# Performance work log

Hardware: AMD Instinct MI355X
Metric: run time of the kernel (lower is better)

Reference implementation:

```python
import jax, jax.numpy as jnp
import numpy as np
import math


def setup_inputs() -> dict:
    key = jax.random.key(0)
    k1, k2, k3 = jax.random.split(key, 3)
    b, h, w = 4, 64, 64
    hw = h * w
    gp_dim = 64
    sim_matrix = jax.random.normal(k1, (b, hw, hw), dtype=jnp.float32)
    conv_w = jax.random.normal(k2, (gp_dim, 2), dtype=jnp.float32)
    conv_b = jax.random.normal(k3, (gp_dim,), dtype=jnp.float32)
    return {"sim_matrix": sim_matrix, "conv_w": conv_w, "conv_b": conv_b,
            "b": b, "h": h, "w": w}


def _pos_enc(conv_w, conv_b, b, h, w):
    # normalized grid coords in (-1, 1), channel 0 = x (width), channel 1 = y (height)
    ys = jnp.linspace(-1.0 + 1.0 / h, 1.0 - 1.0 / h, h, dtype=jnp.float32)
    xs = jnp.linspace(-1.0 + 1.0 / w, 1.0 - 1.0 / w, w, dtype=jnp.float32)
    gy, gx = jnp.meshgrid(ys, xs, indexing="ij")          # [h, w] each
    coords = jnp.stack([gx, gy], axis=0)                   # [2, h, w]
    # 1x1 conv == per-pixel linear: [d,2] @ [2,h,w] + bias
    proj = jnp.einsum("dc,chw->dhw", conv_w, coords) + conv_b[:, None, None]
    f = jnp.cos(8.0 * math.pi * proj)                       # fourier basis, [d, h, w]
    return jnp.broadcast_to(f[None], (b,) + f.shape)        # [b, d, h, w]


def reference(sim_matrix, conv_w, conv_b, b, h, w):
    d = conv_w.shape[0]
    f = _pos_enc(conv_w, conv_b, b, h, w)                   # [b, d, h, w]
    f = f.reshape(b, d, h * w).transpose(0, 2, 1)           # [b, hw, d]
    conf = jax.nn.softmax(sim_matrix, axis=2)               # [b, hw, hw]
    gp = jnp.einsum("bnm,bmd->bnd", conf, f)                # [b, hw, d]
    return gp.transpose(0, 2, 1).reshape(b, d, h, w)        # [b, d, h, w]
```

## Files before the change

### kernel.cpp

```cpp
#include <hip/hip_runtime.h>


typedef _Float16 f16;
typedef f16 f16x8 __attribute__((ext_vector_type(8)));
typedef float f32x4 __attribute__((ext_vector_type(4)));

static constexpr int HW = 4096;
static constexpr int ND = 64;

__global__ __launch_bounds__(256) void posenc_f16(
    const float* __restrict__ cw, const float* __restrict__ cb,
    f16* __restrict__ ft)
{
    int g = blockIdx.x * 256 + threadIdx.x;
    int d = g >> 12;
    int m = g & 4095;
    int i = m >> 6;
    int j = m & 63;
    float gx = (float)(2 * j - 63) * (1.0f / 64.0f);
    float gy = (float)(2 * i - 63) * (1.0f / 64.0f);
    float proj = cw[2 * d] * gx + cw[2 * d + 1] * gy + cb[d];
    float v = cosf(25.132741228718345f * proj);
    ft[(size_t)d * HW + m] = (f16)v;
}

__global__ __launch_bounds__(256) void gp_main(
    const float* __restrict__ sim, const f16* __restrict__ ft,
    float* __restrict__ out)
{
    const int bb   = blockIdx.x >> 6;
    const int nt   = blockIdx.x & 63;
    const int wv   = threadIdx.x >> 6;
    const int lane = threadIdx.x & 63;
    const int c    = lane & 15;
    const int q    = lane >> 4;
    const int n0   = nt * 64 + wv * 16;

    const float* srow  = sim + (size_t)bb * HW * HW + (size_t)(n0 + c) * HW + q * 8;
    const f16*   fbase = ft + (size_t)c * HW + q * 8;

    f32x4 acc0 = {0.f, 0.f, 0.f, 0.f};
    f32x4 acc1 = {0.f, 0.f, 0.f, 0.f};
    f32x4 acc2 = {0.f, 0.f, 0.f, 0.f};
    f32x4 acc3 = {0.f, 0.f, 0.f, 0.f};
    float psum = 0.0f;

    #pragma unroll 2
    for (int m0 = 0; m0 < HW; m0 += 32) {
        f32x4 s0 = *(const f32x4*)(srow + m0);
        f32x4 s1 = *(const f32x4*)(srow + m0 + 4);

        float p0 = __expf(s0[0]);
        float p1 = __expf(s0[1]);
        float p2 = __expf(s0[2]);
        float p3 = __expf(s0[3]);
        float p4 = __expf(s1[0]);
        float p5 = __expf(s1[1]);
        float p6 = __expf(s1[2]);
        float p7 = __expf(s1[3]);
        psum += ((p0 + p1) + (p2 + p3)) + ((p4 + p5) + (p6 + p7));

        f16x8 a;
        a[0] = (f16)p0; a[1] = (f16)p1; a[2] = (f16)p2; a[3] = (f16)p3;
        a[4] = (f16)p4; a[5] = (f16)p5; a[6] = (f16)p6; a[7] = (f16)p7;

        f16x8 b0 = *(const f16x8*)(fbase + (size_t)(0 * 16) * HW + m0);
        f16x8 b1 = *(const f16x8*)(fbase + (size_t)(1 * 16) * HW + m0);
        f16x8 b2 = *(const f16x8*)(fbase + (size_t)(2 * 16) * HW + m0);
        f16x8 b3 = *(const f16x8*)(fbase + (size_t)(3 * 16) * HW + m0);

        acc0 = __builtin_amdgcn_mfma_f32_16x16x32_f16(a, b0, acc0, 0, 0, 0);
        acc1 = __builtin_amdgcn_mfma_f32_16x16x32_f16(a, b1, acc1, 0, 0, 0);
        acc2 = __builtin_amdgcn_mfma_f32_16x16x32_f16(a, b2, acc2, 0, 0, 0);
        acc3 = __builtin_amdgcn_mfma_f32_16x16x32_f16(a, b3, acc3, 0, 0, 0);
    }

    psum += __shfl_xor(psum, 16, 64);
    psum += __shfl_xor(psum, 32, 64);
    float r0 = 1.0f / __shfl(psum, q * 4 + 0, 64);
    float r1 = 1.0f / __shfl(psum, q * 4 + 1, 64);
    float r2 = 1.0f / __shfl(psum, q * 4 + 2, 64);
    float r3 = 1.0f / __shfl(psum, q * 4 + 3, 64);

    float* ob = out + (size_t)bb * ND * HW + (size_t)c * HW + n0 + q * 4;
    {
        f32x4 v; v[0] = acc0[0] * r0; v[1] = acc0[1] * r1; v[2] = acc0[2] * r2; v[3] = acc0[3] * r3;
        *(f32x4*)(ob + (size_t)(0 * 16) * HW) = v;
    }
    {
        f32x4 v; v[0] = acc1[0] * r0; v[1] = acc1[1] * r1; v[2] = acc1[2] * r2; v[3] = acc1[3] * r3;
        *(f32x4*)(ob + (size_t)(1 * 16) * HW) = v;
    }
    {
        f32x4 v; v[0] = acc2[0] * r0; v[1] = acc2[1] * r1; v[2] = acc2[2] * r2; v[3] = acc2[3] * r3;
        *(f32x4*)(ob + (size_t)(2 * 16) * HW) = v;
    }
    {
        f32x4 v; v[0] = acc3[0] * r0; v[1] = acc3[1] * r1; v[2] = acc3[2] * r2; v[3] = acc3[3] * r3;
        *(f32x4*)(ob + (size_t)(3 * 16) * HW) = v;
    }
}

extern "C" void kernel_launch(void* const* d_in, const int* in_sizes, int n_in,
                              void* d_out, int out_size, void* d_ws, size_t ws_size,
                              hipStream_t stream) {
    (void)in_sizes; (void)n_in; (void)out_size; (void)ws_size;
    const float* sim = (const float*)d_in[0];
    const float* cw  = (const float*)d_in[1];
    const float* cb  = (const float*)d_in[2];
    float* out = (float*)d_out;
    f16* ft = (f16*)d_ws;

    posenc_f16<<<(ND * HW) / 256, 256, 0, stream>>>(cw, cb, ft);
    gp_main<<<256, 256, 0, stream>>>(sim, ft, out);
}
```

Baseline: 393.2 us.

## Split softmax-GEMM reduction across eight waves with shared-memory combine

Each block now covers 16 rows instead of 64, and its eight waves each take one eighth of the 4096-wide reduction dimension. Partial MFMA accumulators and exp sums are combined through shared memory before the normalised result is written. This gives 1024 blocks of 512 threads instead of 256 blocks of 256, so more waves are in flight to hide memory latency on the bandwidth-bound stream of the 256MB sim matrix. The cost is a shared-memory reduction, a block barrier, and each wave reading its positional-encoding slice once per block.

```diff
diff --git a/kernel.cpp b/kernel.cpp
--- a/kernel.cpp
+++ b/kernel.cpp
@@ -7,6 +7,8 @@
 
 static constexpr int HW = 4096;
 static constexpr int ND = 64;
+static constexpr int KW = 8;
+static constexpr int KM = HW / KW;
 
 __global__ __launch_bounds__(256) void posenc_f16(
     const float* __restrict__ cw, const float* __restrict__ cb,
@@ -24,20 +26,21 @@
     ft[(size_t)d * HW + m] = (f16)v;
 }
 
-__global__ __launch_bounds__(256) void gp_main(
+__global__ __launch_bounds__(512) void gp_main(
     const float* __restrict__ sim, const f16* __restrict__ ft,
     float* __restrict__ out)
 {
-    const int bb   = blockIdx.x >> 6;
-    const int nt   = blockIdx.x & 63;
+    const int bb   = blockIdx.x >> 8;
+    const int nt   = blockIdx.x & 255;
     const int wv   = threadIdx.x >> 6;
     const int lane = threadIdx.x & 63;
     const int c    = lane & 15;
     const int q    = lane >> 4;
-    const int n0   = nt * 64 + wv * 16;
+    const int n0   = nt * 16;
 
-    const float* srow  = sim + (size_t)bb * HW * HW + (size_t)(n0 + c) * HW + q * 8;
-    const f16*   fbase = ft + (size_t)c * HW + q * 8;
+    const float* srow  = sim + (size_t)bb * HW * HW + (size_t)(n0 + c) * HW
+                             + wv * KM + q * 8;
+    const f16*   fbase = ft + (size_t)c * HW + wv * KM + q * 8;
 
     f32x4 acc0 = {0.f, 0.f, 0.f, 0.f};
     f32x4 acc1 = {0.f, 0.f, 0.f, 0.f};
@@ -45,8 +48,8 @@
     f32x4 acc3 = {0.f, 0.f, 0.f, 0.f};
     float psum = 0.0f;
 
-    #pragma unroll 2
-    for (int m0 = 0; m0 < HW; m0 += 32) {
+    #pragma unroll 4
+    for (int m0 = 0; m0 < KM; m0 += 32) {
         f32x4 s0 = *(const f32x4*)(srow + m0);
         f32x4 s1 = *(const f32x4*)(srow + m0 + 4);
 
@@ -75,29 +78,44 @@
         acc3 = __builtin_amdgcn_mfma_f32_16x16x32_f16(a, b3, acc3, 0, 0, 0);
     }
 
-    psum += __shfl_xor(psum, 16, 64);
-    psum += __shfl_xor(psum, 32, 64);
-    float r0 = 1.0f / __shfl(psum, q * 4 + 0, 64);
-    float r1 = 1.0f / __shfl(psum, q * 4 + 1, 64);
-    float r2 = 1.0f / __shfl(psum, q * 4 + 2, 64);
-    float r3 = 1.0f / __shfl(psum, q * 4 + 3, 64);
+    __shared__ f32x4 red[4][KW][64];
+    __shared__ float redsum[KW][64];
+    red[0][wv][lane] = acc0;
+    red[1][wv][lane] = acc1;
+    red[2][wv][lane] = acc2;
+    red[3][wv][lane] = acc3;
+    redsum[wv][lane] = psum;
+    __syncthreads();
 
-    float* ob = out + (size_t)bb * ND * HW + (size_t)c * HW + n0 + q * 4;
-    {
-        f32x4 v; v[0] = acc0[0] * r0; v[1] = acc0[1] * r1; v[2] = acc0[2] * r2; v[3] = acc0[3] * r3;
-        *(f32x4*)(ob + (size_t)(0 * 16) * HW) = v;
-    }
-    {
-        f32x4 v; v[0] = acc1[0] * r0; v[1] = acc1[1] * r1; v[2] = acc1[2] * r2; v[3] = acc1[3] * r3;
-        *(f32x4*)(ob + (size_t)(1 * 16) * HW) = v;
-    }
-    {
-        f32x4 v; v[0] = acc2[0] * r0; v[1] = acc2[1] * r1; v[2] = acc2[2] * r2; v[3] = acc2[3] * r3;
-        *(f32x4*)(ob + (size_t)(2 * 16) * HW) = v;
-    }
-    {
-        f32x4 v; v[0] = acc3[0] * r0; v[1] = acc3[1] * r1; v[2] = acc3[2] * r2; v[3] = acc3[3] * r3;
-        *(f32x4*)(ob + (size_t)(3 * 16) * HW) = v;
+    if (wv < 2) {
+        const int t0 = wv * 2, t1 = wv * 2 + 1;
+        f32x4 A0 = {0.f, 0.f, 0.f, 0.f};
+        f32x4 A1 = {0.f, 0.f, 0.f, 0.f};
+        float ps = 0.0f;
+        #pragma unroll
+        for (int s = 0; s < KW; s++) {
+            A0 += red[t0][s][lane];
+            A1 += red[t1][s][lane];
+            ps += redsum[s][lane];
+        }
+        ps += __shfl_xor(ps, 16, 64);
+        ps += __shfl_xor(ps, 32, 64);
+        float r0 = 1.0f / __shfl(ps, q * 4 + 0, 64);
+        float r1 = 1.0f / __shfl(ps, q * 4 + 1, 64);
+        float r2 = 1.0f / __shfl(ps, q * 4 + 2, 64);
+        float r3 = 1.0f / __shfl(ps, q * 4 + 3, 64);
+
+        float* ob = out + (size_t)bb * ND * HW + (size_t)c * HW + n0 + q * 4;
+        {
+            f32x4 v; v[0] = A0[0] * r0; v[1] = A0[1] * r1;
+                     v[2] = A0[2] * r2; v[3] = A0[3] * r3;
+            *(f32x4*)(ob + (size_t)t0 * 16 * HW) = v;
+        }
+        {
+            f32x4 v; v[0] = A1[0] * r0; v[1] = A1[1] * r1;
+                     v[2] = A1[2] * r2; v[3] = A1[3] * r3;
+            *(f32x4*)(ob + (size_t)t1 * 16 * HW) = v;
+        }
     }
 }
 
@@ -112,5 +130,5 @@
     f16* ft = (f16*)d_ws;
 
     posenc_f16<<<(ND * HW) / 256, 256, 0, stream>>>(cw, cb, ft);
-    gp_main<<<256, 256, 0, stream>>>(sim, ft, out);
+    gp_main<<<1024, 512, 0, stream>>>(sim, ft, out);
 }
```

New measurement: 384.1 us. -2.3%, faster.

## Stage sim and feature tiles through double-buffered LDS with 8-wave blocks

Applied to the files above, without the earlier changes.

Replaces per-lane strided global reads with cooperative coalesced loads of 64x128 sim tiles and 64x128 feature tiles into double-buffered shared memory, prefetching the next tile into registers while computing. Blocks grow to 8 waves, each handling 16 rows by 32 output channels, so exp is recomputed by two waves per row group. Row sums are combined via shared memory before normalization. This aims to improve memory coalescing and latency hiding at the cost of more LDS usage, barriers, and duplicated exp work.

```diff
diff --git a/kernel.cpp b/kernel.cpp
--- a/kernel.cpp
+++ b/kernel.cpp
@@ -5,8 +5,11 @@
 typedef f16 f16x8 __attribute__((ext_vector_type(8)));
 typedef float f32x4 __attribute__((ext_vector_type(4)));
 
-static constexpr int HW = 4096;
-static constexpr int ND = 64;
+static constexpr int HW  = 4096;
+static constexpr int ND  = 64;
+static constexpr int BK  = 128;
+static constexpr int AST = 132;
+static constexpr int BST = 136;
 
 __global__ __launch_bounds__(256) void posenc_f16(
     const float* __restrict__ cw, const float* __restrict__ cb,
@@ -24,81 +27,124 @@
     ft[(size_t)d * HW + m] = (f16)v;
 }
 
-__global__ __launch_bounds__(256) void gp_main(
+__global__ __launch_bounds__(512, 2) void gp_main(
     const float* __restrict__ sim, const f16* __restrict__ ft,
     float* __restrict__ out)
 {
     const int bb   = blockIdx.x >> 6;
-    const int nt   = blockIdx.x & 63;
-    const int wv   = threadIdx.x >> 6;
-    const int lane = threadIdx.x & 63;
+    const int ng   = blockIdx.x & 63;
+    const int n0   = ng * 64;
+    const int tid  = threadIdx.x;
+    const int wv   = tid >> 6;
+    const int lane = tid & 63;
     const int c    = lane & 15;
     const int q    = lane >> 4;
-    const int n0   = nt * 64 + wv * 16;
+    const int s    = wv & 3;
+    const int h    = wv >> 2;
 
-    const float* srow  = sim + (size_t)bb * HW * HW + (size_t)(n0 + c) * HW + q * 8;
-    const f16*   fbase = ft + (size_t)c * HW + q * 8;
+    __shared__ float As[2][64 * AST];
+    __shared__ f16   Bs[2][64 * BST];
+    __shared__ float Ls[64];
+
+    const float* simb = sim + (size_t)bb * HW * HW + (size_t)n0 * HW;
+
+    const int sr   = tid >> 5;
+    const int sc4  = tid & 31;
+    const int fd   = tid >> 4;
+    const int ft16 = tid & 15;
+
+    f32x4 sreg[4];
+    f16x8 freg[2];
+
+    #define LOAD_TILE(kt)                                                     \
+        {                                                                     \
+            const float* g = simb + (kt) * BK;                                \
+            _Pragma("unroll")                                                 \
+            for (int p = 0; p < 4; p++)                                       \
+                sreg[p] = *(const f32x4*)(g + (size_t)(p * 16 + sr) * HW      \
+                                            + sc4 * 4);                       \
+            const f16* gf = ft + (kt) * BK;                                   \
+            _Pragma("unroll")                                                 \
+            for (int p = 0; p < 2; p++)                                       \
+                freg[p] = *(const f16x8*)(gf + (size_t)(p * 32 + fd) * HW     \
+                                             + ft16 * 8);                     \
+        }
 
     f32x4 acc0 = {0.f, 0.f, 0.f, 0.f};
     f32x4 acc1 = {0.f, 0.f, 0.f, 0.f};
-    f32x4 acc2 = {0.f, 0.f, 0.f, 0.f};
-    f32x4 acc3 = {0.f, 0.f, 0.f, 0.f};
     float psum = 0.0f;
 
-    #pragma unroll 2
-    for (int m0 = 0; m0 < HW; m0 += 32) {
-        f32x4 s0 = *(const f32x4*)(srow + m0);
-        f32x4 s1 = *(const f32x4*)(srow + m0 + 4);
+    LOAD_TILE(0);
 
-        float p0 = __expf(s0[0]);
-        float p1 = __expf(s0[1]);
-        float p2 = __expf(s0[2]);
-        float p3 = __expf(s0[3]);
-        float p4 = __expf(s1[0]);
-        float p5 = __expf(s1[1]);
-        float p6 = __expf(s1[2]);
-        float p7 = __expf(s1[3]);
-        psum += ((p0 + p1) + (p2 + p3)) + ((p4 + p5) + (p6 + p7));
+    for (int kt = 0; kt < HW / BK; kt++) {
+        const int buf = kt & 1;
+        #pragma unroll
+        for (int p = 0; p < 4; p++)
+            *(f32x4*)&As[buf][(p * 16 + sr) * AST + sc4 * 4] = sreg[p];
+        #pragma unroll
+        for (int p = 0; p < 2; p++)
+            *(f16x8*)&Bs[buf][(p * 32 + fd) * BST + ft16 * 8] = freg[p];
+        __syncthreads();
 
-        f16x8 a;
-        a[0] = (f16)p0; a[1] = (f16)p1; a[2] = (f16)p2; a[3] = (f16)p3;
-        a[4] = (f16)p4; a[5] = (f16)p5; a[6] = (f16)p6; a[7] = (f16)p7;
+        if (kt < HW / BK - 1)
+            LOAD_TILE(kt + 1);
 
-        f16x8 b0 = *(const f16x8*)(fbase + (size_t)(0 * 16) * HW + m0);
-        f16x8 b1 = *(const f16x8*)(fbase + (size_t)(1 * 16) * HW + m0);
-        f16x8 b2 = *(const f16x8*)(fbase + (size_t)(2 * 16) * HW + m0);
-        f16x8 b3 = *(const f16x8*)(fbase + (size_t)(3 * 16) * HW + m0);
+        const float* as  = &As[buf][(s * 16 + c) * AST];
+        const f16*   bs0 = &Bs[buf][(h * 32 + c) * BST];
+        const f16*   bs1 = bs0 + 16 * BST;
+        #pragma unroll
+        for (int kk = 0; kk < BK / 32; kk++) {
+            const int ko = kk * 32 + q * 8;
+            f32x4 s0 = *(const f32x4*)(as + ko);
+            f32x4 s1 = *(const f32x4*)(as + ko + 4);
 
-        acc0 = __builtin_amdgcn_mfma_f32_16x16x32_f16(a, b0, acc0, 0, 0, 0);
-        acc1 = __builtin_amdgcn_mfma_f32_16x16x32_f16(a, b1, acc1, 0, 0, 0);
-        acc2 = __builtin_amdgcn_mfma_f32_16x16x32_f16(a, b2, acc2, 0, 0, 0);
-        acc3 = __builtin_amdgcn_mfma_f32_16x16x32_f16(a, b3, acc3, 0, 0, 0);
+            float p0 = __expf(s0[0]);
+            float p1 = __expf(s0[1]);
+            float p2 = __expf(s0[2]);
+            float p3 = __expf(s0[3]);
+            float p4 = __expf(s1[0]);
+            float p5 = __expf(s1[1]);
+            float p6 = __expf(s1[2]);
+            float p7 = __expf(s1[3]);
+            psum += ((p0 + p1) + (p2 + p3)) + ((p4 + p5) + (p6 + p7));
+
+            f16x8 a;
+            a[0] = (f16)p0; a[1] = (f16)p1; a[2] = (f16)p2; a[3] = (f16)p3;
+            a[4] = (f16)p4; a[5] = (f16)p5; a[6] = (f16)p6; a[7] = (f16)p7;
+
+            f16x8 b0 = *(const f16x8*)(bs0 + ko);
+            f16x8 b1 = *(const f16x8*)(bs1 + ko);
+            acc0 = __builtin_amdgcn_mfma_f32_16x16x32_f16(a, b0, acc0, 0, 0, 0);
+            acc1 = __builtin_amdgcn_mfma_f32_16x16x32_f16(a, b1, acc1, 0, 0, 0);
+        }
     }
 
     psum += __shfl_xor(psum, 16, 64);
     psum += __shfl_xor(psum, 32, 64);
-    float r0 = 1.0f / __shfl(psum, q * 4 + 0, 64);
-    float r1 = 1.0f / __shfl(psum, q * 4 + 1, 64);
-    float r2 = 1.0f / __shfl(psum, q * 4 + 2, 64);
-    float r3 = 1.0f / __shfl(psum, q * 4 + 3, 64);
+    if (h == 0 && lane < 16)
+        Ls[s * 16 + lane] = psum;
+    __syncthreads();
 
-    float* ob = out + (size_t)bb * ND * HW + (size_t)c * HW + n0 + q * 4;
+    f32x4 L4 = *(const f32x4*)&Ls[s * 16 + q * 4];
+    float r0 = 1.0f / L4[0];
+    float r1 = 1.0f / L4[1];
+    float r2 = 1.0f / L4[2];
+    float r3 = 1.0f / L4[3];
+
+    float* o0 = out + ((size_t)bb * ND + h * 32 + c) * HW + n0 + s * 16 + q * 4;
     {
-        f32x4 v; v[0] = acc0[0] * r0; v[1] = acc0[1] * r1; v[2] = acc0[2] * r2; v[3] = acc0[3] * r3;
-        *(f32x4*)(ob + (size_t)(0 * 16) * HW) = v;
+        f32x4 v;
+        v[0] = acc0[0] * r0; v[1] = acc0[1] * r1;
+        v[2] = acc0[2] * r2; v[3] = acc0[3] * r3;
+        *(f32x4*)o0 = v;
     }
     {
-        f32x4 v; v[0] = acc1[0] * r0; v[1] = acc1[1] * r1; v[2] = acc1[2] * r2; v[3] = acc1[3] * r3;
-        *(f32x4*)(ob + (size_t)(1 * 16) * HW) = v;
+        f32x4 v;
+        v[0] = acc1[0] * r0; v[1] = acc1[1] * r1;
+        v[2] = acc1[2] * r2; v[3] = acc1[3] * r3;
+        *(f32x4*)(o0 + (size_t)16 * HW) = v;
     }
-    {
-        f32x4 v; v[0] = acc2[0] * r0; v[1] = acc2[1] * r1; v[2] = acc2[2] * r2; v[3] = acc2[3] * r3;
-        *(f32x4*)(ob + (size_t)(2 * 16) * HW) = v;
-    }
-    {
-        f32x4 v; v[0] = acc3[0] * r0; v[1] = acc3[1] * r1; v[2] = acc3[2] * r2; v[3] = acc3[3] * r3;
-        *(f32x4*)(ob + (size_t)(3 * 16) * HW) = v;
-    }
+    #undef LOAD_TILE
 }
 
 extern "C" void kernel_launch(void* const* d_in, const int* in_sizes, int n_in,
@@ -112,5 +158,5 @@
     f16* ft = (f16*)d_ws;
 
     posenc_f16<<<(ND * HW) / 256, 256, 0, stream>>>(cw, cb, ft);
-    gp_main<<<256, 256, 0, stream>>>(sim, ft, out);
+    gp_main<<<256, 512, 0, stream>>>(sim, ft, out);
 }
```

Result: faster. 377.7 us (-4.0%).
